# Optimization experiments

Measured on AMD Instinct MI355X. Metric: run time of the kernel, lower is better.

## Reference

```python
import jax, jax.numpy as jnp
import numpy as np

TAU = 2.0          # LIF tau
V_TH = 1.0         # threshold, v_reset = 0
EPS = 1e-5         # BN eps
NUM_HEADS = 12
PATCH = 4
LENTH = 64         # (H/p)*(W/p)


def _heaviside(x):
    return (x >= 0.0).astype(x.dtype)


def lif(x_seq):
    """Multi-step LIF (decay_input=True, hard reset to 0). x_seq: [T, ...] -> spikes [T, ...]."""
    def step(v, x):
        v = v + (x - v) / TAU
        s = _heaviside(v - V_TH)
        v = v * (1.0 - s)
        return v, s
    _, s_seq = jax.lax.scan(step, jnp.zeros_like(x_seq[0]), x_seq)
    return s_seq


def bn_eval(x, gamma, beta, mean, var):
    # x: [T,B,C,H,W]; eval-mode BN over channel axis 2
    sh = (1, 1, -1, 1, 1)
    inv = gamma.reshape(sh) / jnp.sqrt(var.reshape(sh) + EPS)
    return (x - mean.reshape(sh)) * inv + beta.reshape(sh)


def setup_inputs() -> dict:
    key = jax.random.key(0)
    ks = jax.random.split(key, 8)
    T, B, C, H, W = 4, 8, 384, 32, 32
    p = PATCH
    x = jax.random.normal(ks[0], (T, B, C, H, W), jnp.float32)
    w_conv = jax.random.normal(ks[1], (2 * C, C, p, p), jnp.float32) / np.sqrt(C * p * p)
    w_proj = jax.random.normal(ks[2], (C, C), jnp.float32) / np.sqrt(C)
    bn1_gamma = 0.5 + jax.random.uniform(ks[3], (2 * C,), jnp.float32)
    bn1_beta = 0.1 * jax.random.normal(ks[4], (2 * C,), jnp.float32)
    bn1_mean = 0.1 * jax.random.normal(ks[5], (2 * C,), jnp.float32)
    bn1_var = 0.5 + jax.random.uniform(ks[6], (2 * C,), jnp.float32)
    bn2_gamma = 0.5 + jax.random.uniform(jax.random.fold_in(key, 10), (C,), jnp.float32)
    bn2_beta = 0.1 * jax.random.normal(jax.random.fold_in(key, 11), (C,), jnp.float32)
    bn2_mean = 0.1 * jax.random.normal(jax.random.fold_in(key, 12), (C,), jnp.float32)
    bn2_var = 0.5 + jax.random.uniform(jax.random.fold_in(key, 13), (C,), jnp.float32)
    fr_x = 0.05 + 0.5 * jax.random.uniform(jax.random.fold_in(key, 14), (1, 1, NUM_HEADS, 1, 1), jnp.float32)
    fr_attn = 0.05 + 0.5 * jax.random.uniform(jax.random.fold_in(key, 15), (1, 1, NUM_HEADS, 1, 1), jnp.float32)
    return dict(x=x, w_conv=w_conv, bn1_gamma=bn1_gamma, bn1_beta=bn1_beta,
                bn1_mean=bn1_mean, bn1_var=bn1_var, w_proj=w_proj,
                bn2_gamma=bn2_gamma, bn2_beta=bn2_beta, bn2_mean=bn2_mean,
                bn2_var=bn2_var, fr_x=fr_x, fr_attn=fr_attn)


def reference(x, w_conv, bn1_gamma, bn1_beta, bn1_mean, bn1_var, w_proj,
              bn2_gamma, bn2_beta, bn2_mean, bn2_var, fr_x, fr_attn):
    T, B, C, H, W = x.shape
    h = NUM_HEADS
    Ch = C // h
    p = PATCH
    x_feat = x
    xs = lif(x)                                           # [T,B,C,H,W] spikes
    # patchify conv (kernel=stride=p, no bias), flatten T*B for the conv
    y = jax.lax.conv_general_dilated(
        xs.reshape(T * B, C, H, W), w_conv, (p, p), 'VALID',
        dimension_numbers=('NCHW', 'OIHW', 'NCHW'))
    Hp, Wp = H // p, W // p
    y = bn_eval(y.reshape(T, B, 2 * C, Hp, Wp), bn1_gamma, bn1_beta, bn1_mean, bn1_var)
    y = y.reshape(T, B, h, 2 * Ch, Hp * Wp)
    y1, y2 = y[:, :, :, :Ch, :], y[:, :, :, Ch:, :]       # [T,B,h,Ch,N']
    xr = xs.reshape(T, B, h, Ch, H * W)                   # [T,B,h,Ch,N]
    scale1 = 1.0 / jnp.sqrt(fr_x * Ch)                    # [1,1,h,1,1]
    attn = jnp.einsum('tbhdp,tbhdn->tbhpn', y1, xr) * scale1   # [T,B,h,N',N]
    attn = lif(attn)
    scale2 = 1.0 / jnp.sqrt(fr_attn * LENTH)
    out = jnp.einsum('tbhdp,tbhpn->tbhdn', y2, attn) * scale2  # [T,B,h,Ch,N]
    out = lif(out.reshape(T, B, C, H, W))
    out = jnp.einsum('tbchw,oc->tbohw', out, w_proj)      # 1x1 conv, no bias
    out = bn_eval(out, bn2_gamma, bn2_beta, bn2_mean, bn2_var)
    return out + x_feat
```

## Files before the change

kernel.cpp:

```cpp
#include <hip/hip_runtime.h>
#include <math.h>

#define TT 4
#define BB 8
#define CC 384
#define HWN 1024
#define NHEAD 12
#define CHD 32
#define C2 768
#define LL 64
#define KCONV 6144
#define KB_TOT 192
#define MROWS 2048

#define K2INV ((_Float16)4.8828125e-4f)

typedef _Float16 f16x8 __attribute__((ext_vector_type(8)));
typedef _Float16 f16x4 __attribute__((ext_vector_type(4)));
typedef float f32x4 __attribute__((ext_vector_type(4)));

#if defined(__has_builtin)
#if __has_builtin(__builtin_amdgcn_global_load_lds)
#define USE_GLL 1
#endif
#if __has_builtin(__builtin_amdgcn_sched_barrier)
#define HAVE_SCHEDBAR 1
#endif
#if __has_builtin(__builtin_amdgcn_s_setprio)
#define HAVE_SETPRIO 1
#endif
#endif
#ifndef USE_GLL
#define USE_GLL 0
#endif
#ifndef HAVE_SCHEDBAR
#define HAVE_SCHEDBAR 0
#endif
#ifndef HAVE_SETPRIO
#define HAVE_SETPRIO 0
#endif

#if HAVE_SCHEDBAR
#define SCHED_FENCE() __builtin_amdgcn_sched_barrier(0)
#else
#define SCHED_FENCE()
#endif

#if HAVE_SETPRIO
#define PRIO_HI() __builtin_amdgcn_s_setprio(1)
#define PRIO_LO() __builtin_amdgcn_s_setprio(0)
#else
#define PRIO_HI()
#define PRIO_LO()
#endif

#if USE_GLL
typedef __attribute__((address_space(3))) unsigned int lds_uint;
typedef const __attribute__((address_space(1))) unsigned int glob_uint;
__device__ __forceinline__ void load_lds16(const void* g, void* l) {
    __builtin_amdgcn_global_load_lds((glob_uint*)g, (lds_uint*)l, 16, 0, 0);
}
#endif

__global__ __launch_bounds__(256) void k_pack_all(const float* __restrict__ w,
                                                  const float* __restrict__ wp,
                                                  _Float16* __restrict__ W0,
                                                  _Float16* __restrict__ W1,
                                                  _Float16* __restrict__ WpH) {
    __shared__ __align__(16) _Float16 Lh[4096];
    __shared__ __align__(16) _Float16 Ll[4096];
    int b = blockIdx.x;
    int tid = threadIdx.x;
    int r0 = tid >> 3;
    int c4 = (tid & 7) * 4;
    int q = c4 >> 3, j0 = c4 & 7;
    if (b < 1152) {
        int kb = b / 6, nb = b - kb * 6;
#pragma unroll
        for (int ri = 0; ri < 4; ri++) {
            int col = ri * 32 + r0;
            const float* src = w + (size_t)(nb * 128 + col) * KCONV + kb * 32 + c4;
            float4 v = *(const float4*)src;
            float vv[4] = {v.x, v.y, v.z, v.w};
#pragma unroll
            for (int e = 0; e < 4; e++) {
                _Float16 h = (_Float16)vv[e];
                float rem = (vv[e] - (float)h) * 2048.0f;
                Lh[q * 1024 + col * 8 + j0 + e] = h;
                Ll[q * 1024 + col * 8 + j0 + e] = (_Float16)rem;
            }
        }
        __syncthreads();
        size_t o = ((size_t)kb * 6 + nb) * 4096 + tid * 16;
        *(f16x8*)(W0 + o) = *(const f16x8*)&Lh[tid * 16];
        *(f16x8*)(W0 + o + 8) = *(const f16x8*)&Lh[tid * 16 + 8];
        *(f16x8*)(W1 + o) = *(const f16x8*)&Ll[tid * 16];
        *(f16x8*)(W1 + o + 8) = *(const f16x8*)&Ll[tid * 16 + 8];
    } else {
        int bb = b - 1152;
        int kb = bb / 3, ot = bb - kb * 3;
#pragma unroll
        for (int ri = 0; ri < 4; ri++) {
            int col = ri * 32 + r0;
            const float* src = wp + (size_t)(ot * 128 + col) * CC + kb * 32 + c4;
            float4 v = *(const float4*)src;
            float vv[4] = {v.x, v.y, v.z, v.w};
#pragma unroll
            for (int e = 0; e < 4; e++)
                Lh[q * 1024 + col * 8 + j0 + e] = (_Float16)vv[e];
        }
        __syncthreads();
        size_t o = ((size_t)kb * 3 + ot) * 4096 + tid * 16;
        *(f16x8*)(WpH + o) = *(const f16x8*)&Lh[tid * 16];
        *(f16x8*)(WpH + o + 8) = *(const f16x8*)&Lh[tid * 16 + 8];
    }
}

__global__ __launch_bounds__(256) void k_lif1(const float* __restrict__ x,
                                              _Float16* __restrict__ xsC,
                                              _Float16* __restrict__ xsF) {
    __shared__ __align__(16) _Float16 S[4][4][16][8];
    int nt = blockIdx.x & 3, q8 = blockIdx.x >> 2;
    int bh = blockIdx.y;
    int b = bh / NHEAD, hh = bh % NHEAD;
    int tid = threadIdx.x;
    int n = nt * 256 + tid;
    const int stride = BB * CC * HWN;
    int h = n >> 5, w = n & 31;
    int a = h & 3, pj = w >> 2, bp = w & 3;
    int qa = a >> 1;
    int jc = (a & 1) * 4 + bp;
    int rowloc = ((h >> 2) & 1) * 8 + pj;
    size_t base0 = ((size_t)b * CC + hh * 32 + q8 * 8) * HWN + n;
    f16x8 frag[4];
#pragma unroll
    for (int j = 0; j < 8; j++) {
        float v = 0.0f;
        size_t off = base0 + (size_t)j * HWN;
#pragma unroll
        for (int t = 0; t < TT; t++) {
            float xv = x[(size_t)t * stride + off];
            v += (xv - v) * 0.5f;
            float s = (v >= 1.0f) ? 1.0f : 0.0f;
            if (s > 0.0f) v = 0.0f;
            frag[t][j] = (_Float16)s;
        }
    }
#pragma unroll
    for (int t = 0; t < TT; t++) {
        int tb = t * BB + b;
        size_t dst = ((size_t)(tb * NHEAD + hh) * 8 + (n >> 7)) * 4096 + q8 * 1024 + (size_t)(n & 127) * 8;
        *(f16x8*)(xsF + dst) = frag[t];
    }
    int kb0 = hh * 16 + q8 * 4;
    int okb = tid >> 6, oqc = (tid >> 4) & 3, orow = tid & 15;
#pragma unroll
    for (int t = 0; t < TT; t++) {
        __syncthreads();
#pragma unroll
        for (int j = 0; j < 8; j++)
            S[j >> 1][(j & 1) * 2 + qa][rowloc][jc] = frag[t][j];
        __syncthreads();
        int tb = t * BB + b;
        int mt = tb >> 1;
        int row = (tb & 1) * 64 + nt * 16 + orow;
        _Float16* dst = xsC + (size_t)mt * (192 * 4096) + (size_t)(kb0 + okb) * 4096 + oqc * 1024 + (size_t)row * 8;
        *(f16x8*)dst = *(const f16x8*)&S[okb][oqc][orow][0];
    }
}

__global__ __launch_bounds__(256, 3) void k_conv_mfma(const _Float16* __restrict__ xsC,
                                                      const _Float16* __restrict__ W0,
                                                      const _Float16* __restrict__ W1,
                                                      float* __restrict__ P,
                                                      int KS, int kbPerSplit) {
    __shared__ __align__(16) _Float16 As[2][4096];
    __shared__ __align__(16) _Float16 Bh[2][4096];
    __shared__ __align__(16) _Float16 Bl[2][4096];

    int bid = blockIdx.x;
    int s = bid % KS;
    int idx = bid / KS;
    int mt = idx & 15;
    int nt = idx >> 4;
    int kb0 = s * kbPerSplit;
    int tid = threadIdx.x;
    int wave = tid >> 6;
    int lane = tid & 63;
    int l16 = lane & 15, lq = lane >> 4;
    int wr = (wave & 1) * 64, wc = (wave >> 1) * 64;

    f32x4 acc[4][4];
#pragma unroll
    for (int i = 0; i < 4; i++)
#pragma unroll
        for (int j = 0; j < 4; j++) acc[i][j] = (f32x4){0.f, 0.f, 0.f, 0.f};

    const char* aBase = (const char*)xsC + (size_t)mt * (192 * 8192);
    const char* b0Base = (const char*)W0 + (size_t)nt * 8192;
    const char* b1Base = (const char*)W1 + (size_t)nt * 8192;
    int wo = wave * 2048;
    int lo16 = lane * 16;

#if USE_GLL
#define STAGE(buf, kb) do {                                              \
    const char* aS = aBase + (size_t)(kb) * 8192;                        \
    const char* b0S = b0Base + (size_t)(kb) * (6 * 8192);                \
    const char* b1S = b1Base + (size_t)(kb) * (6 * 8192);                \
    load_lds16(aS + wo + lo16, (char*)As[buf] + wo);                     \
    load_lds16(aS + wo + 1024 + lo16, (char*)As[buf] + wo + 1024);       \
    load_lds16(b0S + wo + lo16, (char*)Bh[buf] + wo);                    \
    load_lds16(b0S + wo + 1024 + lo16, (char*)Bh[buf] + wo + 1024);      \
    load_lds16(b1S + wo + lo16, (char*)Bl[buf] + wo);                    \
    load_lds16(b1S + wo + 1024 + lo16, (char*)Bl[buf] + wo + 1024);      \
} while (0)

    STAGE(0, kb0);
    if (kbPerSplit > 1) STAGE(1, kb0 + 1);
    int cur = 0;
    for (int i = 0; i < kbPerSplit; ++i) {
        if (i < kbPerSplit - 1)
            asm volatile("s_waitcnt vmcnt(6)" ::: "memory");
        else
            asm volatile("s_waitcnt vmcnt(0)" ::: "memory");
        __builtin_amdgcn_s_barrier();
        SCHED_FENCE();

        f16x8 wfh[4], wfl[4], sf[4], sfs[4];
#pragma unroll
        for (int fj = 0; fj < 4; fj++)
            sf[fj] = *(const f16x8*)&As[cur][(size_t)(lq * 128 + wr + fj * 16 + l16) * 8];
#pragma unroll
        for (int fi = 0; fi < 4; fi++) {
            wfh[fi] = *(const f16x8*)&Bh[cur][(size_t)(lq * 128 + wc + fi * 16 + l16) * 8];
            wfl[fi] = *(const f16x8*)&Bl[cur][(size_t)(lq * 128 + wc + fi * 16 + l16) * 8];
        }
        asm volatile("s_waitcnt lgkmcnt(0)" ::: "memory");
        SCHED_FENCE();
        __builtin_amdgcn_s_barrier();
        SCHED_FENCE();
        if (i + 2 < kbPerSplit) STAGE(cur, kb0 + i + 2);
        SCHED_FENCE();

#pragma unroll
        for (int fj = 0; fj < 4; fj++) sfs[fj] = sf[fj] * K2INV;
        PRIO_HI();
#pragma unroll
        for (int fi = 0; fi < 4; fi++)
#pragma unroll
            for (int fj = 0; fj < 4; fj++)
                acc[fi][fj] = __builtin_amdgcn_mfma_f32_16x16x32_f16(wfh[fi], sf[fj], acc[fi][fj], 0, 0, 0);
#pragma unroll
        for (int fi = 0; fi < 4; fi++)
#pragma unroll
            for (int fj = 0; fj < 4; fj++)
                acc[fi][fj] = __builtin_amdgcn_mfma_f32_16x16x32_f16(wfl[fi], sfs[fj], acc[fi][fj], 0, 0, 0);
        PRIO_LO();

        cur ^= 1;
    }
#undef STAGE
#else
#define STAGE(buf, kb) do {                                              \
    const char* aS = aBase + (size_t)(kb) * 8192;                        \
    const char* b0S = b0Base + (size_t)(kb) * (6 * 8192);                \
    const char* b1S = b1Base + (size_t)(kb) * (6 * 8192);                \
    _Pragma("unroll")                                                    \
    for (int i_ = 0; i_ < 2; ++i_) {                                     \
        int off_ = wo + i_ * 1024 + lo16;                                \
        *(float4*)((char*)As[buf] + off_) = *(const float4*)(aS + off_); \
        *(float4*)((char*)Bh[buf] + off_) = *(const float4*)(b0S + off_);\
        *(float4*)((char*)Bl[buf] + off_) = *(const float4*)(b1S + off_);\
    }                                                                    \
} while (0)
    STAGE(0, kb0);
    __syncthreads();
    int cur = 0;
    for (int i = 0; i < kbPerSplit; ++i) {
        if (i + 1 < kbPerSplit) STAGE(cur ^ 1, kb0 + i + 1);
        f16x8 wfh[4], wfl[4], sf[4], sfs[4];
#pragma unroll
        for (int fj = 0; fj < 4; fj++) {
            sf[fj] = *(const f16x8*)&As[cur][(size_t)(lq * 128 + wr + fj * 16 + l16) * 8];
            sfs[fj] = sf[fj] * K2INV;
        }
#pragma unroll
        for (int fi = 0; fi < 4; fi++) {
            wfh[fi] = *(const f16x8*)&Bh[cur][(size_t)(lq * 128 + wc + fi * 16 + l16) * 8];
            wfl[fi] = *(const f16x8*)&Bl[cur][(size_t)(lq * 128 + wc + fi * 16 + l16) * 8];
        }
#pragma unroll
        for (int fi = 0; fi < 4; fi++)
#pragma unroll
            for (int fj = 0; fj < 4; fj++)
                acc[fi][fj] = __builtin_amdgcn_mfma_f32_16x16x32_f16(wfh[fi], sf[fj], acc[fi][fj], 0, 0, 0);
#pragma unroll
        for (int fi = 0; fi < 4; fi++)
#pragma unroll
            for (int fj = 0; fj < 4; fj++)
                acc[fi][fj] = __builtin_amdgcn_mfma_f32_16x16x32_f16(wfl[fi], sfs[fj], acc[fi][fj], 0, 0, 0);
        __syncthreads();
        cur ^= 1;
    }
#undef STAGE
#endif

    size_t Pbase = (size_t)s * MROWS * C2;
#pragma unroll
    for (int fi = 0; fi < 4; fi++) {
        int oc0 = nt * 128 + wc + fi * 16 + lq * 4;
#pragma unroll
        for (int fj = 0; fj < 4; fj++) {
            int m = mt * 128 + wr + fj * 16 + l16;
            *(f32x4*)(P + Pbase + (size_t)m * C2 + oc0) = acc[fi][fj];
        }
    }
}

__global__ __launch_bounds__(256) void k_reduce_frag(const float* __restrict__ P,
                                                     const float* __restrict__ g1,
                                                     const float* __restrict__ b1,
                                                     const float* __restrict__ m1,
                                                     const float* __restrict__ v1,
                                                     _Float16* __restrict__ A1,
                                                     _Float16* __restrict__ A2,
                                                     int KS) {
    __shared__ float y2ls[32][66];
    int tb = blockIdx.x / NHEAD, hh = blockIdx.x % NHEAD;
    int tid = threadIdx.x;
    int pp = tid >> 2, cq = (tid & 3) * 16;

    size_t rowbase = ((size_t)tb * 64 + pp) * C2 + hh * 64 + cq;
    float yv[16];
#pragma unroll
    for (int i = 0; i < 16; i++) yv[i] = 0.0f;
    for (int s = 0; s < KS; s++) {
        const float* p = P + (size_t)s * MROWS * C2 + rowbase;
#pragma unroll
        for (int i4 = 0; i4 < 4; i4++) {
            float4 v = *(const float4*)(p + i4 * 4);
            yv[i4 * 4 + 0] += v.x;
            yv[i4 * 4 + 1] += v.y;
            yv[i4 * 4 + 2] += v.z;
            yv[i4 * 4 + 3] += v.w;
        }
    }
#pragma unroll
    for (int i = 0; i < 16; i++) {
        int oc = hh * 64 + cq + i;
        float inv = g1[oc] / sqrtf(v1[oc] + 1e-5f);
        yv[i] = (yv[i] - m1[oc]) * inv + b1[oc];
    }

    size_t reg = (size_t)(tb * NHEAD + hh) * 4096;
    if (cq < 32) {
#pragma unroll
        for (int gi = 0; gi < 2; gi++) {
            int c0 = cq + gi * 8;
            f16x8 h, l;
#pragma unroll
            for (int j = 0; j < 8; j++) {
                float v = yv[gi * 8 + j];
                _Float16 hi = (_Float16)v;
                h[j] = hi;
                l[j] = (_Float16)((v - (float)hi) * 2048.0f);
            }
            size_t a = reg + (size_t)(((pp >> 4) * 4 + (c0 >> 3)) * 128 + (pp & 15) * 8);
            *(f16x8*)(A1 + a) = h;
            *(f16x8*)(A1 + a + 2048) = l;
        }
    } else {
#pragma unroll
        for (int i = 0; i < 16; i++) y2ls[cq - 32 + i][pp] = yv[i];
    }
    __syncthreads();
    int d16 = tid & 15, grp = tid >> 4;
    f16x8 h, l;
#pragma unroll
    for (int j = 0; j < 8; j++) {
        float v = y2ls[(grp >> 3) * 16 + d16][((grp >> 2) & 1) * 32 + (grp & 3) * 8 + j];
        _Float16 hi = (_Float16)v;
        h[j] = hi;
        l[j] = (_Float16)((v - (float)hi) * 2048.0f);
    }
    size_t a = reg + (size_t)((grp * 16 + d16) * 8);
    *(f16x8*)(A2 + a) = h;
    *(f16x8*)(A2 + a + 2048) = l;
}

__global__ __launch_bounds__(256, 3) void k_attn_mfma(const _Float16* __restrict__ xsF,
                                                      const _Float16* __restrict__ A1,
                                                      const _Float16* __restrict__ A2,
                                                      const float* __restrict__ fr_x,
                                                      const float* __restrict__ fr_attn,
                                                      _Float16* __restrict__ OsF) {
    __shared__ __align__(16) _Float16 Bs[4][128][8];
    __shared__ __align__(16) _Float16 Sat[8][128][8];

    int nt = blockIdx.x;
    int bh = blockIdx.y;
    int b = bh / NHEAD, hh = bh % NHEAD;
    int tid = threadIdx.x;
    int w = tid >> 6;
    int lane = tid & 63;
    int l16 = lane & 15, lq = lane >> 4;

    float scale1 = 1.0f / sqrtf(fr_x[hh] * 32.0f);
    float scale2 = 1.0f / sqrtf(fr_attn[hh] * 64.0f);

    float va[8][4];
    float vo[2][2][4];
#pragma unroll
    for (int nf = 0; nf < 8; nf++)
#pragma unroll
        for (int r = 0; r < 4; r++) va[nf][r] = 0.0f;
#pragma unroll
    for (int dt = 0; dt < 2; dt++)
#pragma unroll
        for (int nf = 0; nf < 2; nf++)
#pragma unroll
            for (int r = 0; r < 4; r++) vo[dt][nf][r] = 0.0f;

    for (int t = 0; t < TT; t++) {
        int tb = t * BB + b;
        size_t reg = (size_t)(tb * NHEAD + hh);
        const char* src = (const char*)(xsF + (reg * 8 + nt) * 4096);
#if USE_GLL
        load_lds16(src + tid * 16, (char*)&Bs[0][0][0] + tid * 16);
        load_lds16(src + tid * 16 + 4096, (char*)&Bs[0][0][0] + tid * 16 + 4096);
#else
        *(float4*)((char*)&Bs[0][0][0] + tid * 16) = *(const float4*)(src + tid * 16);
        *(float4*)((char*)&Bs[0][0][0] + tid * 16 + 4096) = *(const float4*)(src + tid * 16 + 4096);
#endif
        const _Float16* a1b = A1 + reg * 4096;
        f16x8 a1h = *(const f16x8*)(a1b + (size_t)(((w * 4 + lq) * 16 + l16) * 8));
        f16x8 a1l = *(const f16x8*)(a1b + 2048 + (size_t)(((w * 4 + lq) * 16 + l16) * 8));
        f16x8 a1ls = a1l * K2INV;
        __syncthreads();

        f32x4 ah[8];
#pragma unroll
        for (int nf = 0; nf < 8; nf++) ah[nf] = (f32x4){0.f, 0.f, 0.f, 0.f};
        PRIO_HI();
#pragma unroll
        for (int nf = 0; nf < 8; nf++) {
            f16x8 bf = *(const f16x8*)&Bs[lq][nf * 16 + l16][0];
            ah[nf] = __builtin_amdgcn_mfma_f32_16x16x32_f16(a1h, bf, ah[nf], 0, 0, 0);
            ah[nf] = __builtin_amdgcn_mfma_f32_16x16x32_f16(a1ls, bf, ah[nf], 0, 0, 0);
        }
        PRIO_LO();
        int pq = w * 2 + (lq >> 1);
#pragma unroll
        for (int nf = 0; nf < 8; nf++) {
            f16x4 sp;
#pragma unroll
            for (int r = 0; r < 4; r++) {
                float a = ah[nf][r] * scale1;
                float v = va[nf][r];
                v += (a - v) * 0.5f;
                float s = (v >= 1.0f) ? 1.0f : 0.0f;
                va[nf][r] = (s > 0.0f) ? 0.0f : v;
                sp[r] = (_Float16)s;
            }
            *(f16x4*)&Sat[pq][nf * 16 + l16][(lq & 1) * 4] = sp;
        }
        __syncthreads();

        const _Float16* a2b = A2 + reg * 4096;
        f32x4 oh[2][2];
#pragma unroll
        for (int dt = 0; dt < 2; dt++)
#pragma unroll
            for (int nf = 0; nf < 2; nf++) oh[dt][nf] = (f32x4){0.f, 0.f, 0.f, 0.f};
        PRIO_HI();
#pragma unroll
        for (int ks = 0; ks < 2; ks++) {
            f16x8 bf0 = *(const f16x8*)&Sat[ks * 4 + lq][w * 32 + l16][0];
            f16x8 bf1 = *(const f16x8*)&Sat[ks * 4 + lq][w * 32 + 16 + l16][0];
#pragma unroll
            for (int dt = 0; dt < 2; dt++) {
                size_t ao = (size_t)(((dt * 8 + ks * 4 + lq) * 16 + l16) * 8);
                f16x8 a2h = *(const f16x8*)(a2b + ao);
                f16x8 a2ls = *(const f16x8*)(a2b + 2048 + ao) * K2INV;
                oh[dt][0] = __builtin_amdgcn_mfma_f32_16x16x32_f16(a2h, bf0, oh[dt][0], 0, 0, 0);
                oh[dt][0] = __builtin_amdgcn_mfma_f32_16x16x32_f16(a2ls, bf0, oh[dt][0], 0, 0, 0);
                oh[dt][1] = __builtin_amdgcn_mfma_f32_16x16x32_f16(a2h, bf1, oh[dt][1], 0, 0, 0);
                oh[dt][1] = __builtin_amdgcn_mfma_f32_16x16x32_f16(a2ls, bf1, oh[dt][1], 0, 0, 0);
            }
        }
        PRIO_LO();
        _Float16* og = OsF + (reg * 8 + nt) * 4096;
#pragma unroll
        for (int dt = 0; dt < 2; dt++)
#pragma unroll
            for (int nf = 0; nf < 2; nf++) {
                f16x4 sp;
#pragma unroll
                for (int r = 0; r < 4; r++) {
                    float a = oh[dt][nf][r] * scale2;
                    float v = vo[dt][nf][r];
                    v += (a - v) * 0.5f;
                    float s = (v >= 1.0f) ? 1.0f : 0.0f;
                    vo[dt][nf][r] = (s > 0.0f) ? 0.0f : v;
                    sp[r] = (_Float16)s;
                }
                int n = w * 32 + nf * 16 + l16;
                *(f16x4*)(og + (size_t)((dt * 2 + (lq >> 1)) * 1024 + n * 8 + (lq & 1) * 4)) = sp;
            }
        __syncthreads();
    }
}

__global__ __launch_bounds__(256, 3) void k_proj_mfma(const _Float16* __restrict__ OsF,
                                                      const _Float16* __restrict__ WpH,
                                                      const float* __restrict__ g2,
                                                      const float* __restrict__ b2,
                                                      const float* __restrict__ m2,
                                                      const float* __restrict__ vv2,
                                                      const float* __restrict__ x,
                                                      float* __restrict__ out) {
    __shared__ __align__(16) _Float16 Bs[2][4096];

    int bid = blockIdx.x;
    int xcd = bid & 7;
    int idx = bid >> 3;
    int tb = xcd * 4 + idx / 24;
    int rem = idx % 24;
    int nt = rem & 7;
    int ot = rem >> 3;
    int tid = threadIdx.x;
    int wave = tid >> 6;
    int lane = tid & 63;
    int l16 = lane & 15, lq = lane >> 4;
    int wn = (wave & 1) * 64, wo = (wave >> 1) * 64;

    f32x4 acc[4][4];
#pragma unroll
    for (int i = 0; i < 4; i++)
#pragma unroll
        for (int j = 0; j < 4; j++) acc[i][j] = (f32x4){0.f, 0.f, 0.f, 0.f};

    const char* bBase = (const char*)(OsF + ((size_t)tb * NHEAD * 8 + nt) * 4096);
    const _Float16* aBase = WpH + (size_t)ot * 4096 + lq * 1024 + (size_t)(wo + l16) * 8;
    int halfo = wave * 2048;
    int lo16 = lane * 16;

#if USE_GLL
#define PSTAGE(buf, kb) do {                                                   \
    const char* bS = bBase + (size_t)(kb) * (8 * 8192);                        \
    load_lds16(bS + halfo + lo16, (char*)Bs[buf] + halfo);                     \
    load_lds16(bS + halfo + 1024 + lo16, (char*)Bs[buf] + halfo + 1024);       \
} while (0)
#else
#define PSTAGE(buf, kb) do {                                                   \
    const char* bS = bBase + (size_t)(kb) * (8 * 8192);                        \
    _Pragma("unroll")                                                          \
    for (int i_ = 0; i_ < 2; ++i_) {                                           \
        int off_ = halfo + i_ * 1024 + lo16;                                   \
        *(float4*)((char*)Bs[buf] + off_) = *(const float4*)(bS + off_);       \
    }                                                                          \
} while (0)
#endif

    f16x8 af[4], afn[4];
#pragma unroll
    for (int fo = 0; fo < 4; fo++) af[fo] = *(const f16x8*)(aBase + (size_t)(fo * 16) * 8);
    PSTAGE(0, 0);
    __syncthreads();

    int cur = 0;
    for (int kb = 0; kb < 12; ++kb) {
        int kbn = (kb + 1 < 12) ? kb + 1 : kb;
        if (kb + 1 < 12) PSTAGE(cur ^ 1, kb + 1);
        const _Float16* an = aBase + (size_t)kbn * (3 * 4096);
#pragma unroll
        for (int fo = 0; fo < 4; fo++) afn[fo] = *(const f16x8*)(an + (size_t)(fo * 16) * 8);

        f16x8 bf[4];
#pragma unroll
        for (int fn = 0; fn < 4; fn++)
            bf[fn] = *(const f16x8*)&Bs[cur][(size_t)(lq * 128 + wn + fn * 16 + l16) * 8];
        PRIO_HI();
#pragma unroll
        for (int fn = 0; fn < 4; fn++)
#pragma unroll
            for (int fo = 0; fo < 4; fo++)
                acc[fn][fo] = __builtin_amdgcn_mfma_f32_16x16x32_f16(bf[fn], af[fo], acc[fn][fo], 0, 0, 0);
        PRIO_LO();

        __syncthreads();
        cur ^= 1;
#pragma unroll
        for (int fo = 0; fo < 4; fo++) af[fo] = afn[fo];
    }
#undef PSTAGE

    size_t orow_base = (size_t)tb * CC * HWN;
#pragma unroll
    for (int fo = 0; fo < 4; fo++) {
        int o = ot * 128 + wo + fo * 16 + l16;
        float inv = g2[o] / sqrtf(vv2[o] + 1e-5f);
        float mu = m2[o];
        float bt = b2[o];
        size_t obase = orow_base + (size_t)o * HWN;
#pragma unroll
        for (int fn = 0; fn < 4; fn++) {
            size_t addr = obase + (size_t)(nt * 128 + wn + fn * 16 + lq * 4);
            float4 xv = *(const float4*)(x + addr);
            f32x4 a = acc[fn][fo];
            float4 ov;
            ov.x = (a[0] - mu) * inv + bt + xv.x;
            ov.y = (a[1] - mu) * inv + bt + xv.y;
            ov.z = (a[2] - mu) * inv + bt + xv.z;
            ov.w = (a[3] - mu) * inv + bt + xv.w;
            *(float4*)(out + addr) = ov;
        }
    }
}

extern "C" void kernel_launch(void* const* d_in, const int* in_sizes, int n_in,
                              void* d_out, int out_size, void* d_ws, size_t ws_size,
                              hipStream_t stream) {
    const float* x = (const float*)d_in[0];
    const float* w_conv = (const float*)d_in[1];
    const float* bn1_gamma = (const float*)d_in[2];
    const float* bn1_beta = (const float*)d_in[3];
    const float* bn1_mean = (const float*)d_in[4];
    const float* bn1_var = (const float*)d_in[5];
    const float* w_proj = (const float*)d_in[6];
    const float* bn2_gamma = (const float*)d_in[7];
    const float* bn2_beta = (const float*)d_in[8];
    const float* bn2_mean = (const float*)d_in[9];
    const float* bn2_var = (const float*)d_in[10];
    const float* fr_x = (const float*)d_in[11];
    const float* fr_attn = (const float*)d_in[12];

    const size_t FRAG = (size_t)16 * 192 * 4096 * 2;
    const size_t AB = (size_t)TT * BB * NHEAD * 4096 * 2;
    const size_t WB = (size_t)KCONV * C2 * 2;
    const size_t WPB = (size_t)CC * CC * 2;
    const size_t PB = (size_t)MROWS * C2 * 4;
    _Float16* xsC = (_Float16*)d_ws;
    _Float16* xsF = (_Float16*)((char*)xsC + FRAG);
    _Float16* OsF = (_Float16*)((char*)xsF + FRAG);
    _Float16* A1 = (_Float16*)((char*)OsF + FRAG);
    _Float16* A2 = (_Float16*)((char*)A1 + AB);
    _Float16* W0 = (_Float16*)((char*)A2 + AB);
    _Float16* W1 = (_Float16*)((char*)W0 + WB);
    _Float16* WpH = (_Float16*)((char*)W1 + WB);
    char* tail = (char*)WpH + WPB;

    int KS;
    float* P;
    if (ws_size >= (size_t)(tail - (char*)d_ws) + 8 * PB) {
        KS = 8;
        P = (float*)tail;
    } else if (ws_size >= (size_t)(tail - (char*)d_ws) + 4 * PB) {
        KS = 4;
        P = (float*)tail;
    } else {
        KS = 2;
        P = (float*)OsF;
    }
    int kbPerSplit = KB_TOT / KS;

    k_pack_all<<<1188, 256, 0, stream>>>(w_conv, w_proj, W0, W1, WpH);
    k_lif1<<<dim3(16, BB * NHEAD), 256, 0, stream>>>(x, xsC, xsF);
    k_conv_mfma<<<96 * KS, 256, 0, stream>>>(xsC, W0, W1, P, KS, kbPerSplit);
    k_reduce_frag<<<32 * NHEAD, 256, 0, stream>>>(P, bn1_gamma, bn1_beta, bn1_mean, bn1_var, A1, A2, KS);
    k_attn_mfma<<<dim3(8, BB * NHEAD), 256, 0, stream>>>(xsF, A1, A2, fr_x, fr_attn, OsF);
    k_proj_mfma<<<768, 256, 0, stream>>>(OsF, WpH, bn2_gamma, bn2_beta, bn2_mean, bn2_var, x, (float*)d_out);
}
```

Measured before the change: 119.9 us.

## Load conv weight fragments directly to registers, staging only activations through LDS

The conv MFMA kernel stops staging the two weight tiles (high and low halves) through shared memory. Each wave now loads its own weight fragments straight from global memory into registers and prefetches the next k-block's fragments one iteration ahead. Only the activation tile remains double-buffered in LDS. The GLL path with explicit waitcnt and the two-stage-deep prefetch is replaced by a single loop using __syncthreads. This cuts LDS traffic and footprint, which may allow more resident blocks, but it duplicates weight reads across the waves sharing the same columns and adds register pressure from the prefetch buffers.

```diff
diff --git a/kernel.cpp b/kernel.cpp
--- a/kernel.cpp
+++ b/kernel.cpp
@@ -23,9 +23,6 @@
 #if __has_builtin(__builtin_amdgcn_global_load_lds)
 #define USE_GLL 1
 #endif
-#if __has_builtin(__builtin_amdgcn_sched_barrier)
-#define HAVE_SCHEDBAR 1
-#endif
 #if __has_builtin(__builtin_amdgcn_s_setprio)
 #define HAVE_SETPRIO 1
 #endif
@@ -33,17 +30,8 @@
 #ifndef USE_GLL
 #define USE_GLL 0
 #endif
-#ifndef HAVE_SCHEDBAR
-#define HAVE_SCHEDBAR 0
-#endif
 #ifndef HAVE_SETPRIO
 #define HAVE_SETPRIO 0
-#endif
-
-#if HAVE_SCHEDBAR
-#define SCHED_FENCE() __builtin_amdgcn_sched_barrier(0)
-#else
-#define SCHED_FENCE()
 #endif
 
 #if HAVE_SETPRIO
@@ -175,8 +163,6 @@
                                                       float* __restrict__ P,
                                                       int KS, int kbPerSplit) {
     __shared__ __align__(16) _Float16 As[2][4096];
-    __shared__ __align__(16) _Float16 Bh[2][4096];
-    __shared__ __align__(16) _Float16 Bl[2][4096];
 
     int bid = blockIdx.x;
     int s = bid % KS;
@@ -197,98 +183,61 @@
         for (int j = 0; j < 4; j++) acc[i][j] = (f32x4){0.f, 0.f, 0.f, 0.f};
 
     const char* aBase = (const char*)xsC + (size_t)mt * (192 * 8192);
-    const char* b0Base = (const char*)W0 + (size_t)nt * 8192;
-    const char* b1Base = (const char*)W1 + (size_t)nt * 8192;
+    const _Float16* bhP = W0 + (size_t)nt * 4096 + lq * 1024 + (size_t)(wc + l16) * 8;
+    const _Float16* blP = W1 + (size_t)nt * 4096 + lq * 1024 + (size_t)(wc + l16) * 8;
     int wo = wave * 2048;
     int lo16 = lane * 16;
 
 #if USE_GLL
-#define STAGE(buf, kb) do {                                              \
+#define STAGE_A(buf, kb) do {                                            \
     const char* aS = aBase + (size_t)(kb) * 8192;                        \
-    const char* b0S = b0Base + (size_t)(kb) * (6 * 8192);                \
-    const char* b1S = b1Base + (size_t)(kb) * (6 * 8192);                \
     load_lds16(aS + wo + lo16, (char*)As[buf] + wo);                     \
     load_lds16(aS + wo + 1024 + lo16, (char*)As[buf] + wo + 1024);       \
-    load_lds16(b0S + wo + lo16, (char*)Bh[buf] + wo);                    \
-    load_lds16(b0S + wo + 1024 + lo16, (char*)Bh[buf] + wo + 1024);      \
-    load_lds16(b1S + wo + lo16, (char*)Bl[buf] + wo);                    \
-    load_lds16(b1S + wo + 1024 + lo16, (char*)Bl[buf] + wo + 1024);      \
 } while (0)
-
-    STAGE(0, kb0);
-    if (kbPerSplit > 1) STAGE(1, kb0 + 1);
-    int cur = 0;
-    for (int i = 0; i < kbPerSplit; ++i) {
-        if (i < kbPerSplit - 1)
-            asm volatile("s_waitcnt vmcnt(6)" ::: "memory");
-        else
-            asm volatile("s_waitcnt vmcnt(0)" ::: "memory");
-        __builtin_amdgcn_s_barrier();
-        SCHED_FENCE();
-
-        f16x8 wfh[4], wfl[4], sf[4], sfs[4];
-#pragma unroll
-        for (int fj = 0; fj < 4; fj++)
-            sf[fj] = *(const f16x8*)&As[cur][(size_t)(lq * 128 + wr + fj * 16 + l16) * 8];
-#pragma unroll
-        for (int fi = 0; fi < 4; fi++) {
-            wfh[fi] = *(const f16x8*)&Bh[cur][(size_t)(lq * 128 + wc + fi * 16 + l16) * 8];
-            wfl[fi] = *(const f16x8*)&Bl[cur][(size_t)(lq * 128 + wc + fi * 16 + l16) * 8];
-        }
-        asm volatile("s_waitcnt lgkmcnt(0)" ::: "memory");
-        SCHED_FENCE();
-        __builtin_amdgcn_s_barrier();
-        SCHED_FENCE();
-        if (i + 2 < kbPerSplit) STAGE(cur, kb0 + i + 2);
-        SCHED_FENCE();
-
-#pragma unroll
-        for (int fj = 0; fj < 4; fj++) sfs[fj] = sf[fj] * K2INV;
-        PRIO_HI();
-#pragma unroll
-        for (int fi = 0; fi < 4; fi++)
-#pragma unroll
-            for (int fj = 0; fj < 4; fj++)
-                acc[fi][fj] = __builtin_amdgcn_mfma_f32_16x16x32_f16(wfh[fi], sf[fj], acc[fi][fj], 0, 0, 0);
-#pragma unroll
-        for (int fi = 0; fi < 4; fi++)
-#pragma unroll
-            for (int fj = 0; fj < 4; fj++)
-                acc[fi][fj] = __builtin_amdgcn_mfma_f32_16x16x32_f16(wfl[fi], sfs[fj], acc[fi][fj], 0, 0, 0);
-        PRIO_LO();
-
-        cur ^= 1;
-    }
-#undef STAGE
 #else
-#define STAGE(buf, kb) do {                                              \
+#define STAGE_A(buf, kb) do {                                            \
     const char* aS = aBase + (size_t)(kb) * 8192;                        \
-    const char* b0S = b0Base + (size_t)(kb) * (6 * 8192);                \
-    const char* b1S = b1Base + (size_t)(kb) * (6 * 8192);                \
     _Pragma("unroll")                                                    \
     for (int i_ = 0; i_ < 2; ++i_) {                                     \
         int off_ = wo + i_ * 1024 + lo16;                                \
         *(float4*)((char*)As[buf] + off_) = *(const float4*)(aS + off_); \
-        *(float4*)((char*)Bh[buf] + off_) = *(const float4*)(b0S + off_);\
-        *(float4*)((char*)Bl[buf] + off_) = *(const float4*)(b1S + off_);\
     }                                                                    \
 } while (0)
-    STAGE(0, kb0);
+#endif
+
+    f16x8 wfh[4], wfl[4], wfhN[4], wflN[4];
+    {
+        const _Float16* bh = bhP + (size_t)kb0 * (6 * 4096);
+        const _Float16* bl = blP + (size_t)kb0 * (6 * 4096);
+#pragma unroll
+        for (int fi = 0; fi < 4; fi++) {
+            wfh[fi] = *(const f16x8*)(bh + fi * 128);
+            wfl[fi] = *(const f16x8*)(bl + fi * 128);
+        }
+    }
+    STAGE_A(0, kb0);
     __syncthreads();
+
     int cur = 0;
     for (int i = 0; i < kbPerSplit; ++i) {
-        if (i + 1 < kbPerSplit) STAGE(cur ^ 1, kb0 + i + 1);
-        f16x8 wfh[4], wfl[4], sf[4], sfs[4];
+        if (i + 1 < kbPerSplit) {
+            STAGE_A(cur ^ 1, kb0 + i + 1);
+            const _Float16* bh = bhP + (size_t)(kb0 + i + 1) * (6 * 4096);
+            const _Float16* bl = blP + (size_t)(kb0 + i + 1) * (6 * 4096);
+#pragma unroll
+            for (int fi = 0; fi < 4; fi++) {
+                wfhN[fi] = *(const f16x8*)(bh + fi * 128);
+                wflN[fi] = *(const f16x8*)(bl + fi * 128);
+            }
+        }
+
+        f16x8 sf[4], sfs[4];
 #pragma unroll
         for (int fj = 0; fj < 4; fj++) {
             sf[fj] = *(const f16x8*)&As[cur][(size_t)(lq * 128 + wr + fj * 16 + l16) * 8];
             sfs[fj] = sf[fj] * K2INV;
         }
-#pragma unroll
-        for (int fi = 0; fi < 4; fi++) {
-            wfh[fi] = *(const f16x8*)&Bh[cur][(size_t)(lq * 128 + wc + fi * 16 + l16) * 8];
-            wfl[fi] = *(const f16x8*)&Bl[cur][(size_t)(lq * 128 + wc + fi * 16 + l16) * 8];
-        }
+        PRIO_HI();
 #pragma unroll
         for (int fi = 0; fi < 4; fi++)
 #pragma unroll
@@ -299,11 +248,19 @@
 #pragma unroll
             for (int fj = 0; fj < 4; fj++)
                 acc[fi][fj] = __builtin_amdgcn_mfma_f32_16x16x32_f16(wfl[fi], sfs[fj], acc[fi][fj], 0, 0, 0);
+        PRIO_LO();
+
         __syncthreads();
         cur ^= 1;
-    }
-#undef STAGE
-#endif
+        if (i + 1 < kbPerSplit) {
+#pragma unroll
+            for (int fi = 0; fi < 4; fi++) {
+                wfh[fi] = wfhN[fi];
+                wfl[fi] = wflN[fi];
+            }
+        }
+    }
+#undef STAGE_A
 
     size_t Pbase = (size_t)s * MROWS * C2;
 #pragma unroll
```

Measured after the change: 128.6 us. +7.3%, slower.

## Double-buffer attention LDS tiles and drop per-step barriers in LIF1 transpose

Applied to the files above, without the earlier changes.

The attention kernel now double-buffers the spike tile and the attention-spike scratch in shared memory, so the load for the next timestep is issued before the current step's MFMA work. This removes one of the three barriers per step. The LIF1 kernel stages all four timesteps into a larger shared buffer with a single barrier, replacing two barriers per timestep. Shared memory use grows in both kernels, which may lower occupancy, and the correctness of the attention kernel depends on the single remaining barrier ordering the buffer reuse.

```diff
diff --git a/kernel.cpp b/kernel.cpp
--- a/kernel.cpp
+++ b/kernel.cpp
@@ -119,7 +119,7 @@
 __global__ __launch_bounds__(256) void k_lif1(const float* __restrict__ x,
                                               _Float16* __restrict__ xsC,
                                               _Float16* __restrict__ xsF) {
-    __shared__ __align__(16) _Float16 S[4][4][16][8];
+    __shared__ __align__(16) _Float16 S[4][4][4][16][8];
     int nt = blockIdx.x & 3, q8 = blockIdx.x >> 2;
     int bh = blockIdx.y;
     int b = bh / NHEAD, hh = bh % NHEAD;
@@ -152,20 +152,21 @@
         size_t dst = ((size_t)(tb * NHEAD + hh) * 8 + (n >> 7)) * 4096 + q8 * 1024 + (size_t)(n & 127) * 8;
         *(f16x8*)(xsF + dst) = frag[t];
     }
+#pragma unroll
+    for (int t = 0; t < TT; t++)
+#pragma unroll
+        for (int j = 0; j < 8; j++)
+            S[t][j >> 1][(j & 1) * 2 + qa][rowloc][jc] = frag[t][j];
+    __syncthreads();
     int kb0 = hh * 16 + q8 * 4;
     int okb = tid >> 6, oqc = (tid >> 4) & 3, orow = tid & 15;
 #pragma unroll
     for (int t = 0; t < TT; t++) {
-        __syncthreads();
-#pragma unroll
-        for (int j = 0; j < 8; j++)
-            S[j >> 1][(j & 1) * 2 + qa][rowloc][jc] = frag[t][j];
-        __syncthreads();
         int tb = t * BB + b;
         int mt = tb >> 1;
         int row = (tb & 1) * 64 + nt * 16 + orow;
         _Float16* dst = xsC + (size_t)mt * (192 * 4096) + (size_t)(kb0 + okb) * 4096 + oqc * 1024 + (size_t)row * 8;
-        *(f16x8*)dst = *(const f16x8*)&S[okb][oqc][orow][0];
+        *(f16x8*)dst = *(const f16x8*)&S[t][okb][oqc][orow][0];
     }
 }
 
@@ -394,8 +395,8 @@
                                                       const float* __restrict__ fr_x,
                                                       const float* __restrict__ fr_attn,
                                                       _Float16* __restrict__ OsF) {
-    __shared__ __align__(16) _Float16 Bs[4][128][8];
-    __shared__ __align__(16) _Float16 Sat[8][128][8];
+    __shared__ __align__(16) _Float16 Bs[2][4096];
+    __shared__ __align__(16) _Float16 Sat[2][8192];
 
     int nt = blockIdx.x;
     int bh = blockIdx.y;
@@ -421,22 +422,32 @@
 #pragma unroll
             for (int r = 0; r < 4; r++) vo[dt][nf][r] = 0.0f;
 
+#if USE_GLL
+#define ASTAGE(buf, treg) do {                                                        \
+    const char* src_ = (const char*)(xsF + ((size_t)(treg) * 8 + nt) * 4096);         \
+    load_lds16(src_ + tid * 16, (char*)Bs[buf] + tid * 16);                           \
+    load_lds16(src_ + tid * 16 + 4096, (char*)Bs[buf] + tid * 16 + 4096);             \
+} while (0)
+#else
+#define ASTAGE(buf, treg) do {                                                        \
+    const char* src_ = (const char*)(xsF + ((size_t)(treg) * 8 + nt) * 4096);         \
+    *(float4*)((char*)Bs[buf] + tid * 16) = *(const float4*)(src_ + tid * 16);        \
+    *(float4*)((char*)Bs[buf] + tid * 16 + 4096) = *(const float4*)(src_ + tid * 16 + 4096); \
+} while (0)
+#endif
+
+    ASTAGE(0, (size_t)(0 * BB + b) * NHEAD + hh);
+    __syncthreads();
+
+    int cur = 0;
     for (int t = 0; t < TT; t++) {
         int tb = t * BB + b;
         size_t reg = (size_t)(tb * NHEAD + hh);
-        const char* src = (const char*)(xsF + (reg * 8 + nt) * 4096);
-#if USE_GLL
-        load_lds16(src + tid * 16, (char*)&Bs[0][0][0] + tid * 16);
-        load_lds16(src + tid * 16 + 4096, (char*)&Bs[0][0][0] + tid * 16 + 4096);
-#else
-        *(float4*)((char*)&Bs[0][0][0] + tid * 16) = *(const float4*)(src + tid * 16);
-        *(float4*)((char*)&Bs[0][0][0] + tid * 16 + 4096) = *(const float4*)(src + tid * 16 + 4096);
-#endif
         const _Float16* a1b = A1 + reg * 4096;
         f16x8 a1h = *(const f16x8*)(a1b + (size_t)(((w * 4 + lq) * 16 + l16) * 8));
         f16x8 a1l = *(const f16x8*)(a1b + 2048 + (size_t)(((w * 4 + lq) * 16 + l16) * 8));
         f16x8 a1ls = a1l * K2INV;
-        __syncthreads();
+        if (t + 1 < TT) ASTAGE(cur ^ 1, (size_t)((t + 1) * BB + b) * NHEAD + hh);
 
         f32x4 ah[8];
 #pragma unroll
@@ -444,7 +455,7 @@
         PRIO_HI();
 #pragma unroll
         for (int nf = 0; nf < 8; nf++) {
-            f16x8 bf = *(const f16x8*)&Bs[lq][nf * 16 + l16][0];
+            f16x8 bf = *(const f16x8*)&Bs[cur][(size_t)(nf * 16 + l16) * 8 + lq * 1024];
             ah[nf] = __builtin_amdgcn_mfma_f32_16x16x32_f16(a1h, bf, ah[nf], 0, 0, 0);
             ah[nf] = __builtin_amdgcn_mfma_f32_16x16x32_f16(a1ls, bf, ah[nf], 0, 0, 0);
         }
@@ -462,7 +473,7 @@
                 va[nf][r] = (s > 0.0f) ? 0.0f : v;
                 sp[r] = (_Float16)s;
             }
-            *(f16x4*)&Sat[pq][nf * 16 + l16][(lq & 1) * 4] = sp;
+            *(f16x4*)&Sat[cur][(size_t)(pq * 128 + nf * 16 + l16) * 8 + (lq & 1) * 4] = sp;
         }
         __syncthreads();
 
@@ -475,8 +486,8 @@
         PRIO_HI();
 #pragma unroll
         for (int ks = 0; ks < 2; ks++) {
-            f16x8 bf0 = *(const f16x8*)&Sat[ks * 4 + lq][w * 32 + l16][0];
-            f16x8 bf1 = *(const f16x8*)&Sat[ks * 4 + lq][w * 32 + 16 + l16][0];
+            f16x8 bf0 = *(const f16x8*)&Sat[cur][(size_t)((ks * 4 + lq) * 128 + w * 32 + l16) * 8];
+            f16x8 bf1 = *(const f16x8*)&Sat[cur][(size_t)((ks * 4 + lq) * 128 + w * 32 + 16 + l16) * 8];
 #pragma unroll
             for (int dt = 0; dt < 2; dt++) {
                 size_t ao = (size_t)(((dt * 8 + ks * 4 + lq) * 16 + l16) * 8);
@@ -507,8 +518,9 @@
                 int n = w * 32 + nf * 16 + l16;
                 *(f16x4*)(og + (size_t)((dt * 2 + (lq >> 1)) * 1024 + n * 8 + (lq & 1) * 4)) = sp;
             }
-        __syncthreads();
-    }
+        cur ^= 1;
+    }
+#undef ASTAGE
 }
 
 __global__ __launch_bounds__(256, 3) void k_proj_mfma(const _Float16* __restrict__ OsF,
```

After: 121.7 us. Within noise of the previous version (+1.6%).
